# Performance work log

Hardware: AMD Instinct MI355X
Metric: run time of the kernel (lower is better)

The kernel has to match this reference:

```python
import jax, jax.numpy as jnp
import numpy as np

SCALES = [1.0, 0.9, 0.8, 0.7, 0.6]  # [1 - i/10 for i in range(level=5)]
RES_SCALE = 1.0


def conv2d(x, w, b, pad):
    # NCHW conv, OIHW weights, stride 1, symmetric padding
    y = jax.lax.conv_general_dilated(
        x, w, window_strides=(1, 1), padding=[(pad, pad), (pad, pad)],
        dimension_numbers=("NCHW", "OIHW", "NCHW"))
    return y + b[None, :, None, None]


def _cubic_kernel(d, a=-0.75):
    # torch-style bicubic kernel (a = -0.75)
    d = jnp.abs(d)
    w1 = ((a + 2.0) * d - (a + 3.0)) * d * d + 1.0          # |d| <= 1
    w2 = (((a * d) - 5.0 * a) * d + 8.0 * a) * d - 4.0 * a  # 1 < |d| < 2
    return jnp.where(d <= 1.0, w1, jnp.where(d < 2.0, w2, 0.0))


def _resize_axis(x, out_size, axis):
    in_size = x.shape[axis]
    scale = in_size / out_size
    src = (jnp.arange(out_size, dtype=jnp.float32) + 0.5) * scale - 0.5  # align_corners=False
    x0 = jnp.floor(src)
    t = src - x0
    x0 = x0.astype(jnp.int32)
    out = 0.0
    bshape = [1] * x.ndim
    bshape[axis] = out_size
    for off in range(-1, 3):
        idx = jnp.clip(x0 + off, 0, in_size - 1)  # border replicate
        wgt = _cubic_kernel(t - off).reshape(bshape)
        out = out + jnp.take(x, idx, axis=axis) * wgt
    return out


def bicubic(x, oh, ow):
    return _resize_axis(_resize_axis(x, oh, 2), ow, 3)


def setup_inputs() -> dict:
    key = jax.random.key(0)
    ks = jax.random.split(key, 7)
    C, Cr = 64, 32  # channel=64, reduction=2
    x = jax.random.normal(ks[0], (4, C, 48, 48), dtype=jnp.float32)
    wb = jax.random.normal(ks[1], (Cr, C, 3, 3), dtype=jnp.float32) * 0.05  # conv_match_L_base
    bb = jax.random.normal(ks[2], (Cr,), dtype=jnp.float32) * 0.05
    wm = jax.random.normal(ks[3], (Cr, C, 3, 3), dtype=jnp.float32) * 0.05  # conv_match
    bm = jax.random.normal(ks[4], (Cr,), dtype=jnp.float32) * 0.05
    wa = jax.random.normal(ks[5], (C, C, 1, 1), dtype=jnp.float32) * 0.05   # conv_assembly
    ba = jax.random.normal(ks[6], (C,), dtype=jnp.float32) * 0.05
    return {"x": x, "wb": wb, "bb": bb, "wm": wm, "bm": bm, "wa": wa, "ba": ba}


def reference(x, wb, bb, wm, bm, wa, ba):
    N, C, H, W = x.shape
    mb = conv2d(x, wb, bb, 1)                           # [N,Cr,H,W]
    Cr = mb.shape[1]
    mb = mb.reshape(N, Cr, H * W).transpose(0, 2, 1)    # [N,HW,Cr]  (queries)
    raws, keys = [], []
    for s in SCALES:
        ref = x if s == 1.0 else bicubic(x, int(H * s), int(W * s))
        raws.append(conv2d(ref, wa, ba, 0).reshape(N, C, -1))   # values [N,C,HiWi]
        keys.append(conv2d(ref, wm, bm, 1).reshape(N, Cr, -1))  # keys   [N,Cr,HiWi]
    pyr = jnp.concatenate(keys, axis=-1)                        # [N,Cr,L]
    raw = jnp.concatenate(raws, axis=-1).transpose(0, 2, 1)     # [N,L,C]
    score = jax.nn.softmax(jnp.einsum("nqc,ncl->nql", mb, pyr), axis=-1)  # [N,HW,L]
    y = jnp.einsum("nql,nlc->nqc", score, raw)                  # [N,HW,C]
    y = y.transpose(0, 2, 1).reshape(N, C, H, W)
    return y * RES_SCALE + x
```

## Files before the change

### kernel.cpp

```cpp
#include <hip/hip_runtime.h>
#include <math.h>

typedef unsigned short ushort_t;
typedef __attribute__((ext_vector_type(8))) short short8;
typedef __attribute__((ext_vector_type(4))) float float4v;

#define NB 4
#define C 64
#define CR 32
#define HW 2304
#define LTOT 7470
#define LPAD 7472
#define NSEG 8
#define SEG 960
#define LOG2E 1.44269504088896f

#define YP_F 0
#define LP_F 4718592
#define MBBF_F   4792320
#define KEYBF_F  4939776
#define RAWTBF_F 5417856
#define WPK_F    6374272
#define WPQ_F    6383488
#define WPV_F    6392704

static __device__ __forceinline__ ushort_t f2bf(float f) {
  union { float f; unsigned u; } v; v.f = f;
  unsigned r = v.u + 0x7FFF + ((v.u >> 16) & 1);
  return (ushort_t)(r >> 16);
}

__device__ __forceinline__ float cubicw(float d) {
  float ad = fabsf(d);
  float w1 = (1.25f * ad - 2.25f) * ad * ad + 1.0f;
  float w2 = ((-0.75f * ad + 3.75f) * ad - 6.0f) * ad + 3.0f;
  return ad <= 1.0f ? w1 : (ad < 2.0f ? w2 : 0.0f);
}

__global__ void k_zero(ushort_t* __restrict__ xt) {
  int i = blockIdx.x * 256 + threadIdx.x;
  if (i < 264000) {
    uint4 z = {0u, 0u, 0u, 0u};
    *(uint4*)(xt + (size_t)i * 8) = z;
  }
}

__global__ __launch_bounds__(256) void k_pad0(const float* __restrict__ x,
                                              ushort_t* __restrict__ xt) {
  __shared__ float tile[64][49];
  int py = blockIdx.x, n = blockIdx.y, t = threadIdx.x;
#pragma unroll
  for (int i = 0; i < 12; i++) {
    int idx = i * 256 + t;
    int c = idx / 48, px = idx % 48;
    tile[c][px] = x[(size_t)(n * 64 + c) * HW + py * 48 + px];
  }
  __syncthreads();
#pragma unroll
  for (int i = 0; i < 12; i++) {
    int idx = i * 256 + t;
    int c = idx & 63, px = idx >> 6;
    xt[(size_t)(n * 2500 + (py + 1) * 50 + px + 1) * 64 + c] = f2bf(tile[c][px]);
  }
}

__global__ void k_resize(const float* __restrict__ x, ushort_t* __restrict__ xt) {
  int tid = blockIdx.x * 256 + threadIdx.x;
  int D, Dp, PDD, rem, pixb;
  if (tid < 473344)       { D = 43; Dp = 45; PDD = 2025; rem = tid;           pixb = 10000; }
  else if (tid < 843008)  { D = 38; Dp = 40; PDD = 1600; rem = tid - 473344;  pixb = 18100; }
  else if (tid < 1121792) { D = 33; Dp = 35; PDD = 1225; rem = tid - 843008;  pixb = 24500; }
  else                    { D = 28; Dp = 30; PDD = 900;  rem = tid - 1121792; pixb = 29400; }
  int DD = D * D;
  int pix = rem % DD, nc = rem / DD;
  int py = pix / D, px = pix % D;
  float scale = 48.0f / (float)D;
  float sy = ((float)py + 0.5f) * scale - 0.5f;
  float sx = ((float)px + 0.5f) * scale - 0.5f;
  float y0f = floorf(sy), x0f = floorf(sx);
  int y0 = (int)y0f, x0 = (int)x0f;
  float ty = sy - y0f, tx = sx - x0f;
  float wy[4], wxv[4];
#pragma unroll
  for (int k = 0; k < 4; k++) {
    wy[k]  = cubicw(ty - (float)(k - 1));
    wxv[k] = cubicw(tx - (float)(k - 1));
  }
  const float* src = x + (size_t)nc * HW;
  float acc = 0.f;
#pragma unroll
  for (int dy = 0; dy < 4; ++dy) {
    int iy = min(max(y0 - 1 + dy, 0), 47);
    const float* row = src + iy * 48;
    float a = 0.f;
#pragma unroll
    for (int dx = 0; dx < 4; ++dx) {
      int ix = min(max(x0 - 1 + dx, 0), 47);
      a = fmaf(wxv[dx], row[ix], a);
    }
    acc = fmaf(wy[dy], a, acc);
  }
  int n = nc >> 6, c = nc & 63;
  xt[(size_t)(pixb + n * PDD + (py + 1) * Dp + (px + 1)) * 64 + c] = f2bf(acc);
}

__global__ void k_wpack(const float* __restrict__ wm, const float* __restrict__ wb,
                        const float* __restrict__ wa, ushort_t* __restrict__ wpk,
                        ushort_t* __restrict__ wpq, ushort_t* __restrict__ wpv) {
  int tid = blockIdx.x * 256 + threadIdx.x;
  if (tid >= 5120) return;
  int lane = tid & 63, col = lane & 15, kg = lane >> 4;
  if (tid < 4608) {
    int f = (tid >> 6) % 36;
    bool isq = tid >= 2304;
    int tap = f >> 2, half = (f >> 1) & 1, crt = f & 1;
    int cr = crt * 16 + col;
    int ic0 = half * 32 + kg * 8;
    const float* w = isq ? wb : wm;
    short8 v;
#pragma unroll
    for (int j = 0; j < 8; j++) v[j] = (short)f2bf(w[cr * 576 + (ic0 + j) * 9 + tap]);
    *(short8*)((isq ? wpq : wpk) + (size_t)f * 512 + lane * 8) = v;
  } else {
    int id = tid - 4608;
    int f = id >> 6;
    int half = f >> 2, vt = f & 3;
    int c = vt * 16 + col, ic0 = half * 32 + kg * 8;
    short8 v;
#pragma unroll
    for (int j = 0; j < 8; j++) v[j] = (short)f2bf(wa[c * 64 + ic0 + j]);
    *(short8*)(wpv + (size_t)f * 512 + lane * 8) = v;
  }
}

__global__ __launch_bounds__(256) void k_conv(const ushort_t* __restrict__ xt,
    const ushort_t* __restrict__ wpk, const ushort_t* __restrict__ wpq,
    const ushort_t* __restrict__ wpv, const float* __restrict__ bm,
    const float* __restrict__ bb, const float* __restrict__ ba,
    ushort_t* __restrict__ keybf, ushort_t* __restrict__ mbbf,
    ushort_t* __restrict__ rawtbf) {
  int t = threadIdx.x;
  int unit = blockIdx.x * 4 + (t >> 6);
  if (unit >= 938) return;
  int lane = t & 63, col = lane & 15, quad = lane >> 4;
  int n = blockIdx.y;
  int tile = unit >> 1, crt = unit & 1;
  int D, Dp, PDD, DD, pixb, lb, tloc;
  if (tile < 144)      { D = 48; Dp = 50; PDD = 2500; DD = 2304; pixb = 0;     lb = 0;    tloc = tile; }
  else if (tile < 260) { D = 43; Dp = 45; PDD = 2025; DD = 1849; pixb = 10000; lb = 2304; tloc = tile - 144; }
  else if (tile < 351) { D = 38; Dp = 40; PDD = 1600; DD = 1444; pixb = 18100; lb = 4153; tloc = tile - 260; }
  else if (tile < 420) { D = 33; Dp = 35; PDD = 1225; DD = 1089; pixb = 24500; lb = 5597; tloc = tile - 351; }
  else                 { D = 28; Dp = 30; PDD = 900;  DD = 784;  pixb = 29400; lb = 6686; tloc = tile - 420; }
  bool lvl0 = (tile < 144);

  int p = tloc * 16 + col;
  int pv = min(p, DD - 1);
  int py = pv / D, px = pv - py * D;
  const ushort_t* xb = xt + ((size_t)(pixb + n * PDD + (py + 1) * Dp + (px + 1))) * 64 + quad * 8;

  float4v Dk = {0.f, 0.f, 0.f, 0.f};
  float4v Dq = {0.f, 0.f, 0.f, 0.f};
  float4v Dv0 = {0.f, 0.f, 0.f, 0.f};
  float4v Dv1 = {0.f, 0.f, 0.f, 0.f};

#pragma unroll
  for (int dy = -1; dy <= 1; dy++) {
#pragma unroll
    for (int dx = -1; dx <= 1; dx++) {
      int tap = (dy + 1) * 3 + (dx + 1);
      const ushort_t* ab = xb + (dy * Dp + dx) * 64;
#pragma unroll
      for (int half = 0; half < 2; half++) {
        short8 A = *(const short8*)(ab + half * 32);
        int f = (tap * 2 + half) * 2 + crt;
        short8 Bk = *(const short8*)(wpk + (size_t)f * 512 + lane * 8);
        Dk = __builtin_amdgcn_mfma_f32_16x16x32_bf16(A, Bk, Dk, 0, 0, 0);
        if (lvl0) {
          short8 Bq = *(const short8*)(wpq + (size_t)f * 512 + lane * 8);
          Dq = __builtin_amdgcn_mfma_f32_16x16x32_bf16(A, Bq, Dq, 0, 0, 0);
        }
        if (tap == 4) {
          short8 Bv0 = *(const short8*)(wpv + (size_t)(half * 4 + crt * 2) * 512 + lane * 8);
          short8 Bv1 = *(const short8*)(wpv + (size_t)(half * 4 + crt * 2 + 1) * 512 + lane * 8);
          Dv0 = __builtin_amdgcn_mfma_f32_16x16x32_bf16(A, Bv0, Dv0, 0, 0, 0);
          Dv1 = __builtin_amdgcn_mfma_f32_16x16x32_bf16(A, Bv1, Dv1, 0, 0, 0);
        }
      }
    }
  }

  float biask = bm[crt * 16 + col];
  float biasq = bb[crt * 16 + col];
  float biasv0 = ba[crt * 32 + col];
  float biasv1 = ba[crt * 32 + 16 + col];
  int prow = tloc * 16 + quad * 4;
#pragma unroll
  for (int r = 0; r < 4; r++) {
    if (prow + r < DD) {
      int l = lb + prow + r;
      keybf[(size_t)(n * LTOT + l) * 32 + crt * 16 + col] = f2bf(Dk[r] + biask);
      if (lvl0) mbbf[(size_t)(n * HW + l) * 32 + crt * 16 + col] = f2bf((Dq[r] + biasq) * LOG2E);
      rawtbf[(size_t)(n * 64 + crt * 32 + col) * LPAD + l] = f2bf(Dv0[r] + biasv0);
      rawtbf[(size_t)(n * 64 + crt * 32 + 16 + col) * LPAD + l] = f2bf(Dv1[r] + biasv1);
    }
  }
}

__global__ __launch_bounds__(256) void k_attn(const ushort_t* __restrict__ mb,
    const ushort_t* __restrict__ keyb, const ushort_t* __restrict__ rawt,
    float* __restrict__ Yp, float* __restrict__ lp) {
  __shared__ __align__(16) ushort_t KsF[2048];
  __shared__ __align__(16) ushort_t VsF[4096];
  __shared__ __align__(16) ushort_t Pl[4 * 1152];

  int t = threadIdx.x;
  int n = blockIdx.y, seg = blockIdx.z;
  int lane = t & 63, wv = t >> 6;
  int col = lane & 15, quad = lane >> 4;
  int qb = blockIdx.x * 64 + wv * 16;
  int l_begin = seg * SEG;
  int l_end = min(l_begin + SEG, LTOT);
  int nfull = (l_end - l_begin) >> 6;
  int rem = (l_end - l_begin) & 63;

  short8 qA = *(const short8*)(mb + ((size_t)(n * HW + qb + col)) * CR + quad * 8);

  float4v Y[4];
#pragma unroll
  for (int ct = 0; ct < 4; ct++)
#pragma unroll
    for (int r = 0; r < 4; r++) Y[ct][r] = 0.f;
  float ls[4] = {0.f, 0.f, 0.f, 0.f};

  ushort_t* Pw = Pl + wv * 1152;
  const ushort_t* keyn = keyb + (size_t)n * LTOT * CR;
  const ushort_t* rawn = rawt + (size_t)n * C * LPAD;
  const float4v zero4 = {0.f, 0.f, 0.f, 0.f};

  int kl_off = ((t >> 6) << 4) + (t & 15);
  int kg = (t >> 4) & 3;

  for (int ch = 0; ch <= nfull; ++ch) {
    bool tail = (ch == nfull);
    if (tail && rem == 0) break;
    int l0 = l_begin + ch * 64;

    *(uint4*)&KsF[t * 8] =
        *(const uint4*)(keyn + ((size_t)(l0 + kl_off)) * CR + kg * 8);
#pragma unroll
    for (int i = 0; i < 2; i++) {
      int v = t + (i << 8);
      int kt = v >> 8, ct = (v >> 6) & 3, g = (v >> 4) & 3, cc = v & 15;
      *(uint4*)&VsF[v * 8] =
          *(const uint4*)(rawn + ((size_t)(ct * 16 + cc)) * LPAD + l0 + kt * 32 + g * 8);
    }
    __syncthreads();

#pragma unroll
    for (int tt = 0; tt < 4; tt++) {
      short8 bK = *(const short8*)&KsF[(tt * 64 + lane) * 8];
      float4v S = __builtin_amdgcn_mfma_f32_16x16x32_bf16(qA, bK, zero4, 0, 0, 0);
      bool ok = !tail || (tt * 16 + col < rem);
#pragma unroll
      for (int r = 0; r < 4; r++) {
        float p = __builtin_amdgcn_exp2f(S[r]);
        p = ok ? p : 0.f;
        ls[r] += p;
        union { float f; unsigned u; } cv; cv.f = p;
        Pw[(quad * 4 + r) * 72 + tt * 16 + col] = (ushort_t)((cv.u + 0x8000u) >> 16);
      }
    }
    __syncthreads();

#pragma unroll
    for (int kt = 0; kt < 2; kt++) {
      short8 aP = *(const short8*)&Pw[col * 72 + kt * 32 + quad * 8];
#pragma unroll
      for (int ct = 0; ct < 4; ct++) {
        short8 bV = *(const short8*)&VsF[(((kt << 2) | ct) * 64 + lane) * 8];
        Y[ct] = __builtin_amdgcn_mfma_f32_16x16x32_bf16(aP, bV, Y[ct], 0, 0, 0);
      }
    }
    __syncthreads();
  }

#pragma unroll
  for (int off = 1; off < 16; off <<= 1)
#pragma unroll
    for (int r = 0; r < 4; r++) ls[r] += __shfl_xor(ls[r], off);

  float* yo = Yp + ((size_t)(seg * NB + n) * HW + qb) * C;
#pragma unroll
  for (int ct = 0; ct < 4; ct++)
#pragma unroll
    for (int r = 0; r < 4; r++)
      yo[(quad * 4 + r) * C + ct * 16 + col] = Y[ct][r];
  if (col == 0) {
    int base = (seg * NB + n) * HW + qb + quad * 4;
#pragma unroll
    for (int r = 0; r < 4; r++) lp[base + r] = ls[r];
  }
}

__global__ void k_combine(const float* __restrict__ x, const float* __restrict__ ws,
                          float* __restrict__ out) {
  int tid = blockIdx.x * 256 + threadIdx.x;
  int c = tid & 63;
  int t2 = tid >> 6;
  int q = t2 % HW;
  int n = t2 / HW;
  const float* Yv = ws + YP_F;
  const float* lpv = ws + LP_F;
  int i0 = n * HW + q;
  float den = 0.f, num = 0.f;
#pragma unroll
  for (int s = 0; s < NSEG; s++) {
    int idx = s * NB * HW + i0;
    den += lpv[idx];
    num += Yv[(size_t)idx * C + c];
  }
  int oi = (n * C + c) * HW + q;
  out[oi] = num / den + x[oi];
}

extern "C" void kernel_launch(void* const* d_in, const int* in_sizes, int n_in,
                              void* d_out, int out_size, void* d_ws, size_t ws_size,
                              hipStream_t stream) {
  const float* x  = (const float*)d_in[0];
  const float* wb = (const float*)d_in[1];
  const float* bb = (const float*)d_in[2];
  const float* wm = (const float*)d_in[3];
  const float* bm = (const float*)d_in[4];
  const float* wa = (const float*)d_in[5];
  const float* ba = (const float*)d_in[6];
  float* out = (float*)d_out;
  float* ws = (float*)d_ws;
  ushort_t* xt     = (ushort_t*)ws;
  ushort_t* mbbf   = (ushort_t*)(ws + MBBF_F);
  ushort_t* keybf  = (ushort_t*)(ws + KEYBF_F);
  ushort_t* rawtbf = (ushort_t*)(ws + RAWTBF_F);
  ushort_t* wpk    = (ushort_t*)(ws + WPK_F);
  ushort_t* wpq    = (ushort_t*)(ws + WPQ_F);
  ushort_t* wpv    = (ushort_t*)(ws + WPV_F);

  k_zero<<<1032, 256, 0, stream>>>(xt);
  k_pad0<<<dim3(48, 4), 256, 0, stream>>>(x, xt);
  k_resize<<<5166, 256, 0, stream>>>(x, xt);
  k_wpack<<<20, 256, 0, stream>>>(wm, wb, wa, wpk, wpq, wpv);
  k_conv<<<dim3(235, 4), 256, 0, stream>>>(xt, wpk, wpq, wpv, bm, bb, ba,
                                           keybf, mbbf, rawtbf);
  k_attn<<<dim3(36, 4, NSEG), 256, 0, stream>>>(mbbf, keybf, rawtbf,
      ws + YP_F, ws + LP_F);
  k_combine<<<2304, 256, 0, stream>>>(x, ws, out);
}
```

Measured before the change: 156.7 us.

## Restructure attention kernel: 32 queries per wave, double-buffered V, direct K loads

```diff
diff --git a/kernel.cpp b/kernel.cpp
--- a/kernel.cpp
+++ b/kernel.cpp
@@ -11,18 +11,18 @@
 #define HW 2304
 #define LTOT 7470
 #define LPAD 7472
-#define NSEG 8
-#define SEG 960
+#define NSEG 15
+#define SEG 512
 #define LOG2E 1.44269504088896f
 
 #define YP_F 0
-#define LP_F 4718592
-#define MBBF_F   4792320
-#define KEYBF_F  4939776
-#define RAWTBF_F 5417856
-#define WPK_F    6374272
-#define WPQ_F    6383488
-#define WPV_F    6392704
+#define LP_F 8847360
+#define MBBF_F   8985600
+#define KEYBF_F  9133056
+#define RAWTBF_F 9611136
+#define WPK_F    10567552
+#define WPQ_F    10576768
+#define WPV_F    10585984
 
 static __device__ __forceinline__ ushort_t f2bf(float f) {
   union { float f; unsigned u; } v; v.f = f;
@@ -206,99 +206,117 @@
   }
 }
 
-__global__ __launch_bounds__(256) void k_attn(const ushort_t* __restrict__ mb,
+__global__ __launch_bounds__(256, 4) void k_attn(const ushort_t* __restrict__ mb,
     const ushort_t* __restrict__ keyb, const ushort_t* __restrict__ rawt,
     float* __restrict__ Yp, float* __restrict__ lp) {
-  __shared__ __align__(16) ushort_t KsF[2048];
-  __shared__ __align__(16) ushort_t VsF[4096];
-  __shared__ __align__(16) ushort_t Pl[4 * 1152];
+  __shared__ __align__(16) ushort_t VsF[2][4096];
+  __shared__ __align__(16) ushort_t Pq[4][32 * 72];
 
   int t = threadIdx.x;
   int n = blockIdx.y, seg = blockIdx.z;
   int lane = t & 63, wv = t >> 6;
   int col = lane & 15, quad = lane >> 4;
-  int qb = blockIdx.x * 64 + wv * 16;
+  int qb = blockIdx.x * 128 + wv * 32;
   int l_begin = seg * SEG;
   int l_end = min(l_begin + SEG, LTOT);
   int nfull = (l_end - l_begin) >> 6;
   int rem = (l_end - l_begin) & 63;
-
-  short8 qA = *(const short8*)(mb + ((size_t)(n * HW + qb + col)) * CR + quad * 8);
-
-  float4v Y[4];
-#pragma unroll
-  for (int ct = 0; ct < 4; ct++)
-#pragma unroll
-    for (int r = 0; r < 4; r++) Y[ct][r] = 0.f;
-  float ls[4] = {0.f, 0.f, 0.f, 0.f};
-
-  ushort_t* Pw = Pl + wv * 1152;
+  int nch = nfull + (rem ? 1 : 0);
+
   const ushort_t* keyn = keyb + (size_t)n * LTOT * CR;
   const ushort_t* rawn = rawt + (size_t)n * C * LPAD;
+
+  short8 qA0 = *(const short8*)(mb + ((size_t)(n * HW + qb + col)) * CR + quad * 8);
+  short8 qA1 = *(const short8*)(mb + ((size_t)(n * HW + qb + 16 + col)) * CR + quad * 8);
+
+  int ct0 = (t >> 6) & 3, g0 = (t >> 4) & 3, cc0 = t & 15;
+  size_t so0 = (size_t)(ct0 * 16 + cc0) * LPAD + g0 * 8;
+
+  float4v Y0[4], Y1[4];
+#pragma unroll
+  for (int ct = 0; ct < 4; ct++)
+#pragma unroll
+    for (int r = 0; r < 4; r++) { Y0[ct][r] = 0.f; Y1[ct][r] = 0.f; }
+  float ls0 = 0.f, ls1 = 0.f;
   const float4v zero4 = {0.f, 0.f, 0.f, 0.f};
-
-  int kl_off = ((t >> 6) << 4) + (t & 15);
-  int kg = (t >> 4) & 3;
-
-  for (int ch = 0; ch <= nfull; ++ch) {
-    bool tail = (ch == nfull);
-    if (tail && rem == 0) break;
+  ushort_t* Pw = Pq[wv];
+
+  uint4 va = *(const uint4*)(rawn + so0 + l_begin);
+  uint4 vb = *(const uint4*)(rawn + so0 + 32 + l_begin);
+  int buf = 0;
+
+  for (int ch = 0; ch < nch; ++ch) {
     int l0 = l_begin + ch * 64;
-
-    *(uint4*)&KsF[t * 8] =
-        *(const uint4*)(keyn + ((size_t)(l0 + kl_off)) * CR + kg * 8);
-#pragma unroll
-    for (int i = 0; i < 2; i++) {
-      int v = t + (i << 8);
-      int kt = v >> 8, ct = (v >> 6) & 3, g = (v >> 4) & 3, cc = v & 15;
-      *(uint4*)&VsF[v * 8] =
-          *(const uint4*)(rawn + ((size_t)(ct * 16 + cc)) * LPAD + l0 + kt * 32 + g * 8);
+    *(uint4*)&VsF[buf][t * 8] = va;
+    *(uint4*)&VsF[buf][(t + 256) * 8] = vb;
+    if (ch + 1 < nch) {
+      int ln = l0 + 64;
+      va = *(const uint4*)(rawn + so0 + ln);
+      vb = *(const uint4*)(rawn + so0 + 32 + ln);
     }
     __syncthreads();
 
+    bool tail = (rem != 0) && (ch == nfull);
 #pragma unroll
     for (int tt = 0; tt < 4; tt++) {
-      short8 bK = *(const short8*)&KsF[(tt * 64 + lane) * 8];
-      float4v S = __builtin_amdgcn_mfma_f32_16x16x32_bf16(qA, bK, zero4, 0, 0, 0);
-      bool ok = !tail || (tt * 16 + col < rem);
+      short8 kf = *(const short8*)(keyn + (size_t)(l0 + tt * 16 + col) * CR + quad * 8);
+      float4v S0 = __builtin_amdgcn_mfma_f32_16x16x32_bf16(kf, qA0, zero4, 0, 0, 0);
+      float4v S1 = __builtin_amdgcn_mfma_f32_16x16x32_bf16(kf, qA1, zero4, 0, 0, 0);
+      int lbase = tt * 16 + quad * 4;
+      float p0[4], p1[4];
 #pragma unroll
       for (int r = 0; r < 4; r++) {
-        float p = __builtin_amdgcn_exp2f(S[r]);
-        p = ok ? p : 0.f;
-        ls[r] += p;
-        union { float f; unsigned u; } cv; cv.f = p;
-        Pw[(quad * 4 + r) * 72 + tt * 16 + col] = (ushort_t)((cv.u + 0x8000u) >> 16);
+        bool ok = !tail || (lbase + r < rem);
+        float a = __builtin_amdgcn_exp2f(S0[r]);
+        float b = __builtin_amdgcn_exp2f(S1[r]);
+        p0[r] = ok ? a : 0.f;
+        p1[r] = ok ? b : 0.f;
+        ls0 += p0[r];
+        ls1 += p1[r];
       }
-    }
-    __syncthreads();
+      union { float f; unsigned u; } c0, c1;
+      uint2 w;
+      c0.f = p0[0]; c1.f = p0[1];
+      w.x = ((c0.u + 0x8000u) >> 16) | ((c1.u + 0x8000u) & 0xFFFF0000u);
+      c0.f = p0[2]; c1.f = p0[3];
+      w.y = ((c0.u + 0x8000u) >> 16) | ((c1.u + 0x8000u) & 0xFFFF0000u);
+      *(uint2*)&Pw[col * 72 + lbase] = w;
+      c0.f = p1[0]; c1.f = p1[1];
+      w.x = ((c0.u + 0x8000u) >> 16) | ((c1.u + 0x8000u) & 0xFFFF0000u);
+      c0.f = p1[2]; c1.f = p1[3];
+      w.y = ((c0.u + 0x8000u) >> 16) | ((c1.u + 0x8000u) & 0xFFFF0000u);
+      *(uint2*)&Pw[(16 + col) * 72 + lbase] = w;
+    }
 
 #pragma unroll
     for (int kt = 0; kt < 2; kt++) {
-      short8 aP = *(const short8*)&Pw[col * 72 + kt * 32 + quad * 8];
+      short8 a0 = *(const short8*)&Pw[col * 72 + kt * 32 + quad * 8];
+      short8 a1 = *(const short8*)&Pw[(16 + col) * 72 + kt * 32 + quad * 8];
 #pragma unroll
       for (int ct = 0; ct < 4; ct++) {
-        short8 bV = *(const short8*)&VsF[(((kt << 2) | ct) * 64 + lane) * 8];
-        Y[ct] = __builtin_amdgcn_mfma_f32_16x16x32_bf16(aP, bV, Y[ct], 0, 0, 0);
+        short8 bV = *(const short8*)&VsF[buf][(((kt << 2) | ct) * 64 + lane) * 8];
+        Y0[ct] = __builtin_amdgcn_mfma_f32_16x16x32_bf16(a0, bV, Y0[ct], 0, 0, 0);
+        Y1[ct] = __builtin_amdgcn_mfma_f32_16x16x32_bf16(a1, bV, Y1[ct], 0, 0, 0);
       }
     }
-    __syncthreads();
-  }
-
-#pragma unroll
-  for (int off = 1; off < 16; off <<= 1)
-#pragma unroll
-    for (int r = 0; r < 4; r++) ls[r] += __shfl_xor(ls[r], off);
+    buf ^= 1;
+  }
+
+  ls0 += __shfl_xor(ls0, 16); ls0 += __shfl_xor(ls0, 32);
+  ls1 += __shfl_xor(ls1, 16); ls1 += __shfl_xor(ls1, 32);
 
   float* yo = Yp + ((size_t)(seg * NB + n) * HW + qb) * C;
 #pragma unroll
   for (int ct = 0; ct < 4; ct++)
 #pragma unroll
-    for (int r = 0; r < 4; r++)
-      yo[(quad * 4 + r) * C + ct * 16 + col] = Y[ct][r];
-  if (col == 0) {
-    int base = (seg * NB + n) * HW + qb + quad * 4;
-#pragma unroll
-    for (int r = 0; r < 4; r++) lp[base + r] = ls[r];
+    for (int r = 0; r < 4; r++) {
+      yo[(quad * 4 + r) * C + ct * 16 + col] = Y0[ct][r];
+      yo[(16 + quad * 4 + r) * C + ct * 16 + col] = Y1[ct][r];
+    }
+  if (quad == 0) {
+    int base = (seg * NB + n) * HW + qb;
+    lp[base + col] = ls0;
+    lp[base + 16 + col] = ls1;
   }
 }
 
@@ -349,7 +367,7 @@
   k_wpack<<<20, 256, 0, stream>>>(wm, wb, wa, wpk, wpq, wpv);
   k_conv<<<dim3(235, 4), 256, 0, stream>>>(xt, wpk, wpq, wpv, bm, bb, ba,
                                            keybf, mbbf, rawtbf);
-  k_attn<<<dim3(36, 4, NSEG), 256, 0, stream>>>(mbbf, keybf, rawtbf,
+  k_attn<<<dim3(18, 4, NSEG), 256, 0, stream>>>(mbbf, keybf, rawtbf,
       ws + YP_F, ws + LP_F);
   k_combine<<<2304, 256, 0, stream>>>(x, ws, out);
 }
```

New measurement: 154.1 us. About the same (-1.6%).
